# Kernel optimization log

Hardware: AMD Instinct MI355X
Metric: run time of the kernel (lower is better)

The kernel has to match this reference:

```python
import jax, jax.numpy as jnp
import numpy as np

N_IN, N_OUT, M, K, CIN, COUT = 262144, 393216, 262144, 27, 32, 64
BN_EPS = 1e-5


def setup_inputs() -> dict:
    key = jax.random.key(0)
    k0, k1, k2, k3 = jax.random.split(key, 4)
    data = jax.random.normal(k0, (N_IN, CIN), dtype=jnp.float32)
    # Kaiming-like scale for conv weights over K*Cin fan-in
    W = jax.random.normal(k1, (K, CIN, COUT), dtype=jnp.float32) * (1.0 / np.sqrt(K * CIN))
    gamma = jnp.ones((COUT,), dtype=jnp.float32)
    beta = jnp.zeros((COUT,), dtype=jnp.float32)
    in_idx = jax.random.randint(k2, (K, M), 0, N_IN, dtype=jnp.int32)
    out_idx = jax.random.randint(k3, (K, M), 0, N_OUT, dtype=jnp.int32)
    return {"data": data, "W": W, "gamma": gamma, "beta": beta,
            "in_idx": in_idx, "out_idx": out_idx}


def _sparse_conv(data, W, in_idx, out_idx):
    # Rulebook sparse conv: for each kernel offset k, gather -> matmul -> scatter-add.
    def step(acc, xs):
        in_i, out_i, Wk = xs              # [M], [M], [CIN, COUT]
        gathered = data[in_i]             # [M, CIN]
        contrib = gathered @ Wk           # [M, COUT]
        return acc.at[out_i].add(contrib), None

    out0 = jnp.zeros((N_OUT, COUT), dtype=data.dtype)
    out, _ = jax.lax.scan(step, out0, (in_idx, out_idx, W))
    return out


def _batch_norm(x, gamma, beta):
    # Sparse batch norm: per-channel stats over all active voxels (training mode).
    mean = jnp.mean(x, axis=0)
    var = jnp.var(x, axis=0)
    inv = jax.lax.rsqrt(var + BN_EPS)
    return (x - mean) * inv * gamma + beta


def reference(data, W, gamma, beta, in_idx, out_idx):
    conv_out = _sparse_conv(data, W, in_idx, out_idx)  # [N_OUT, COUT]
    return _batch_norm(conv_out, gamma, beta)
```

## Files before the change

### kernel.cpp

```cpp
#include <hip/hip_runtime.h>

#define N_IN   262144
#define N_OUT  393216
#define M_PAIRS 262144
#define KK     27
#define CIN    32
#define COUT   64
#define BN_EPS 1e-5f

#define BPK 256
#define PAIRS_PER_BLOCK (M_PAIRS / BPK)
#define CONV_BLOCK 256
#define WAVES_PER_BLOCK (CONV_BLOCK / 64)
#define PAIRS_PER_WAVE (PAIRS_PER_BLOCK / WAVES_PER_BLOCK)

__global__ __launch_bounds__(CONV_BLOCK) void conv_scatter(
    const float* __restrict__ data,
    const float* __restrict__ W,
    const int*   __restrict__ in_idx,
    const int*   __restrict__ out_idx,
    float*       __restrict__ out)
{
    __shared__ float Wlds[CIN * COUT];
    const int k   = blockIdx.x / BPK;
    const int blk = blockIdx.x % BPK;

    for (int i = threadIdx.x; i < CIN * COUT; i += CONV_BLOCK)
        Wlds[i] = W[k * CIN * COUT + i];
    __syncthreads();

    const int wave = threadIdx.x >> 6;
    const int lane = threadIdx.x & 63;
    const int base = k * M_PAIRS + blk * PAIRS_PER_BLOCK + wave * PAIRS_PER_WAVE;

    for (int p = 0; p < PAIRS_PER_WAVE; ++p) {
        const int in_i  = in_idx[base + p];
        const int out_i = out_idx[base + p];
        const float val = data[in_i * CIN + (lane & 31)];
        float acc = 0.0f;
        #pragma unroll
        for (int c = 0; c < CIN; ++c) {
            const float rowv = __shfl(val, c, 64);
            acc = fmaf(rowv, Wlds[c * COUT + lane], acc);
        }
        atomicAdd(&out[out_i * COUT + lane], acc);
    }
}

__global__ __launch_bounds__(256) void bn_stats(
    const float* __restrict__ out, float* __restrict__ stats )
{
    const int tid    = blockIdx.x * 256 + threadIdx.x;
    const int stride = gridDim.x * 256;
    float s = 0.0f, sq = 0.0f;
    const int total = N_OUT * COUT;
    for (int i = tid; i < total; i += stride) {
        const float x = out[i];
        s += x;
        sq += x * x;
    }
    __shared__ float ls[256], lsq[256];
    ls[threadIdx.x]  = s;
    lsq[threadIdx.x] = sq;
    __syncthreads();
    const int c = threadIdx.x;
    if (c < 64) {
        const float ts = ls[c] + ls[c + 64] + ls[c + 128] + ls[c + 192];
        const float tq = lsq[c] + lsq[c + 64] + lsq[c + 128] + lsq[c + 192];
        atomicAdd(&stats[c], ts);
        atomicAdd(&stats[64 + c], tq);
    }
}

__global__ __launch_bounds__(256) void bn_norm(
    float* __restrict__ out, const float* __restrict__ stats,
    const float* __restrict__ gamma, const float* __restrict__ beta)
{
    __shared__ float scale[COUT], bias[COUT];
    if (threadIdx.x < COUT) {
        const int c = threadIdx.x;
        const float invN = 1.0f / (float)N_OUT;
        const float mean = stats[c] * invN;
        const float var  = stats[64 + c] * invN - mean * mean;
        const float inv  = rsqrtf(var + BN_EPS);
        const float g    = gamma[c];
        scale[c] = inv * g;
        bias[c]  = beta[c] - mean * inv * g;
    }
    __syncthreads();

    const int tid    = blockIdx.x * blockDim.x + threadIdx.x;
    const int stride = gridDim.x * blockDim.x;
    const int total4 = N_OUT * COUT / 4;
    float4* o4 = (float4*)out;
    for (int i = tid; i < total4; i += stride) {
        float4 v = o4[i];
        const int c0 = (i * 4) & 63;
        v.x = v.x * scale[c0 + 0] + bias[c0 + 0];
        v.y = v.y * scale[c0 + 1] + bias[c0 + 1];
        v.z = v.z * scale[c0 + 2] + bias[c0 + 2];
        v.w = v.w * scale[c0 + 3] + bias[c0 + 3];
        o4[i] = v;
    }
}

extern "C" void kernel_launch(void* const* d_in, const int* in_sizes, int n_in,
                              void* d_out, int out_size, void* d_ws, size_t ws_size,
                              hipStream_t stream) {
    const float* data    = (const float*)d_in[0];
    const float* W       = (const float*)d_in[1];
    const float* gamma   = (const float*)d_in[2];
    const float* beta    = (const float*)d_in[3];
    const int*   in_idx  = (const int*)d_in[4];
    const int*   out_idx = (const int*)d_in[5];
    float* out   = (float*)d_out;
    float* stats = (float*)d_ws;

    hipMemsetAsync(d_out, 0, (size_t)N_OUT * COUT * sizeof(float), stream);
    hipMemsetAsync(d_ws, 0, 128 * sizeof(float), stream);

    conv_scatter<<<KK * BPK, CONV_BLOCK, 0, stream>>>(data, W, in_idx, out_idx, out);
    bn_stats<<<1024, 256, 0, stream>>>(out, stats);
    bn_norm<<<2048, 256, 0, stream>>>(out, stats, gamma, beta);
}
```

Before: 2.503 ms.

## Bin rulebook by output row range and accumulate in LDS with fused BN stats

Builds a counting-sort of rulebook entries keyed by (output row block, kernel offset): count, single-block prefix scan, then scatter packed records. Each block then owns 128 output rows, accumulates all contributions in shared memory with LDS atomics, computes BN partial statistics directly, and writes its tile once, removing global atomics, the output memset and the separate stats pass. The cost is extra passes over the index arrays, a serial one-block scan over about 80K bins, and only 3072 blocks with heavy LDS use. A fallback to the old path is kept for when the workspace is too small.

Measured after the change: 5.665 ms. 2.26x slower.

```diff
diff --git a/kernel.cpp b/kernel.cpp
--- a/kernel.cpp
+++ b/kernel.cpp
@@ -1,75 +1,139 @@
 #include <hip/hip_runtime.h>
 
-#define N_IN   262144
-#define N_OUT  393216
+#define N_IN    262144
+#define N_OUT   393216
 #define M_PAIRS 262144
-#define KK     27
-#define CIN    32
-#define COUT   64
-#define BN_EPS 1e-5f
-
-#define BPK 256
-#define PAIRS_PER_BLOCK (M_PAIRS / BPK)
-#define CONV_BLOCK 256
-#define WAVES_PER_BLOCK (CONV_BLOCK / 64)
-#define PAIRS_PER_WAVE (PAIRS_PER_BLOCK / WAVES_PER_BLOCK)
-
-__global__ __launch_bounds__(CONV_BLOCK) void conv_scatter(
+#define KK      27
+#define CIN     32
+#define COUT    64
+#define BN_EPS  1e-5f
+
+#define TOTAL_E      (KK * M_PAIRS)
+#define ROWS_PER_BIN 128
+#define NR           (N_OUT / ROWS_PER_BIN)
+#define NBINS        (NR * KK)
+
+typedef unsigned int u32;
+
+__global__ __launch_bounds__(256) void bin_count(
+    const int* __restrict__ out_idx, u32* __restrict__ cnt)
+{
+    const int stride = gridDim.x * 256;
+    for (int e = blockIdx.x * 256 + threadIdx.x; e < TOTAL_E; e += stride) {
+        const int k = e >> 18;
+        const int r = out_idx[e] >> 7;
+        atomicAdd(&cnt[r * KK + k], 1u);
+    }
+}
+
+__global__ __launch_bounds__(1024) void scan_bins(
+    u32* __restrict__ cnt, u32* __restrict__ off)
+{
+    __shared__ u32 sh[1024];
+    __shared__ u32 carry;
+    const int t = threadIdx.x;
+    if (t == 0) carry = 0;
+    __syncthreads();
+    for (int chunk = 0; chunk < NBINS / 1024; ++chunk) {
+        const int i = chunk * 1024 + t;
+        const u32 v = cnt[i];
+        sh[t] = v;
+        __syncthreads();
+        #pragma unroll
+        for (int d = 1; d < 1024; d <<= 1) {
+            const u32 add = (t >= d) ? sh[t - d] : 0u;
+            __syncthreads();
+            sh[t] += add;
+            __syncthreads();
+        }
+        const u32 excl = sh[t] - v + carry;
+        off[i] = excl;
+        cnt[i] = excl;
+        __syncthreads();
+        if (t == 1023) carry += sh[1023];
+        __syncthreads();
+    }
+    if (t == 0) off[NBINS] = carry;
+}
+
+__global__ __launch_bounds__(256) void bin_scatter(
+    const int* __restrict__ in_idx, const int* __restrict__ out_idx,
+    u32* __restrict__ cursor, u32* __restrict__ rec)
+{
+    const int stride = gridDim.x * 256;
+    for (int e = blockIdx.x * 256 + threadIdx.x; e < TOTAL_E; e += stride) {
+        const int k    = e >> 18;
+        const int oi   = out_idx[e];
+        const int ii   = in_idx[e];
+        const int bin  = (oi >> 7) * KK + k;
+        const u32 pos  = atomicAdd(&cursor[bin], 1u);
+        rec[pos] = (u32)ii | ((u32)(oi & 127) << 18);
+    }
+}
+
+__global__ __launch_bounds__(256) void range_accum(
     const float* __restrict__ data,
     const float* __restrict__ W,
-    const int*   __restrict__ in_idx,
-    const int*   __restrict__ out_idx,
-    float*       __restrict__ out)
-{
-    __shared__ float Wlds[CIN * COUT];
-    const int k   = blockIdx.x / BPK;
-    const int blk = blockIdx.x % BPK;
-
-    for (int i = threadIdx.x; i < CIN * COUT; i += CONV_BLOCK)
-        Wlds[i] = W[k * CIN * COUT + i];
-    __syncthreads();
-
-    const int wave = threadIdx.x >> 6;
-    const int lane = threadIdx.x & 63;
-    const int base = k * M_PAIRS + blk * PAIRS_PER_BLOCK + wave * PAIRS_PER_WAVE;
-
-    for (int p = 0; p < PAIRS_PER_WAVE; ++p) {
-        const int in_i  = in_idx[base + p];
-        const int out_i = out_idx[base + p];
-        const float val = data[in_i * CIN + (lane & 31)];
-        float acc = 0.0f;
-        #pragma unroll
-        for (int c = 0; c < CIN; ++c) {
-            const float rowv = __shfl(val, c, 64);
-            acc = fmaf(rowv, Wlds[c * COUT + lane], acc);
-        }
-        atomicAdd(&out[out_i * COUT + lane], acc);
-    }
-}
-
-__global__ __launch_bounds__(256) void bn_stats(
-    const float* __restrict__ out, float* __restrict__ stats )
-{
-    const int tid    = blockIdx.x * 256 + threadIdx.x;
-    const int stride = gridDim.x * 256;
-    float s = 0.0f, sq = 0.0f;
-    const int total = N_OUT * COUT;
-    for (int i = tid; i < total; i += stride) {
-        const float x = out[i];
-        s += x;
-        sq += x * x;
-    }
-    __shared__ float ls[256], lsq[256];
-    ls[threadIdx.x]  = s;
-    lsq[threadIdx.x] = sq;
-    __syncthreads();
-    const int c = threadIdx.x;
-    if (c < 64) {
-        const float ts = ls[c] + ls[c + 64] + ls[c + 128] + ls[c + 192];
-        const float tq = lsq[c] + lsq[c + 64] + lsq[c + 128] + lsq[c + 192];
-        atomicAdd(&stats[c], ts);
-        atomicAdd(&stats[64 + c], tq);
-    }
+    const u32*  __restrict__ off,
+    const u32*  __restrict__ rec,
+    float*      __restrict__ out,
+    float*      __restrict__ stats)
+{
+    __shared__ float acc[ROWS_PER_BIN * COUT];
+    __shared__ float Wl[CIN * COUT];
+    const int r    = blockIdx.x;
+    const int tid  = threadIdx.x;
+    const int wave = tid >> 6;
+    const int lane = tid & 63;
+
+    for (int i = tid; i < ROWS_PER_BIN * COUT; i += 256) acc[i] = 0.0f;
+
+    for (int k = 0; k < KK; ++k) {
+        __syncthreads();
+        for (int i = tid; i < CIN * COUT; i += 256)
+            Wl[i] = W[k * CIN * COUT + i];
+        __syncthreads();
+
+        const u32 begin = off[r * KK + k];
+        const u32 end   = off[r * KK + k + 1];
+        for (u32 idx = begin + wave; idx < end; idx += 4) {
+            const u32 rc   = rec[idx];
+            const int in_i = (int)(rc & 0x3FFFFu);
+            const int lo   = (int)(rc >> 18);
+            const float val = data[in_i * CIN + (lane & 31)];
+            float a = 0.0f;
+            #pragma unroll
+            for (int c = 0; c < CIN; ++c) {
+                const float rv = __shfl(val, c, 64);
+                a = fmaf(rv, Wl[c * COUT + lane], a);
+            }
+            atomicAdd(&acc[lo * COUT + lane], a);
+        }
+    }
+    __syncthreads();
+
+    {
+        const int c = tid & 63;
+        float s = 0.0f, sq = 0.0f;
+        for (int row = tid >> 6; row < ROWS_PER_BIN; row += 4) {
+            const float x = acc[row * COUT + c];
+            s += x; sq += x * x;
+        }
+        Wl[tid]       = s;
+        Wl[256 + tid] = sq;
+        __syncthreads();
+        if (tid < 64) {
+            const float ts = Wl[tid] + Wl[tid + 64] + Wl[tid + 128] + Wl[tid + 192];
+            const float tq = Wl[256 + tid] + Wl[320 + tid] + Wl[384 + tid] + Wl[448 + tid];
+            atomicAdd(&stats[tid], ts);
+            atomicAdd(&stats[64 + tid], tq);
+        }
+    }
+
+    const float4* a4 = (const float4*)acc;
+    float4* o4 = (float4*)out;
+    for (int i = tid; i < ROWS_PER_BIN * COUT / 4; i += 256)
+        o4[r * (ROWS_PER_BIN * COUT / 4) + i] = a4[i];
 }
 
 __global__ __launch_bounds__(256) void bn_norm(
@@ -104,6 +168,51 @@
     }
 }
 
+__global__ __launch_bounds__(256) void conv_scatter_fb(
+    const float* __restrict__ data, const float* __restrict__ W,
+    const int* __restrict__ in_idx, const int* __restrict__ out_idx,
+    float* __restrict__ out)
+{
+    __shared__ float Wlds[CIN * COUT];
+    const int k   = blockIdx.x / 256;
+    const int blk = blockIdx.x % 256;
+    for (int i = threadIdx.x; i < CIN * COUT; i += 256)
+        Wlds[i] = W[k * CIN * COUT + i];
+    __syncthreads();
+    const int wave = threadIdx.x >> 6;
+    const int lane = threadIdx.x & 63;
+    const int base = k * M_PAIRS + blk * 1024 + wave * 256;
+    for (int p = 0; p < 256; ++p) {
+        const int in_i  = in_idx[base + p];
+        const int out_i = out_idx[base + p];
+        const float val = data[in_i * CIN + (lane & 31)];
+        float a = 0.0f;
+        #pragma unroll
+        for (int c = 0; c < CIN; ++c)
+            a = fmaf(__shfl(val, c, 64), Wlds[c * COUT + lane], a);
+        atomicAdd(&out[out_i * COUT + lane], a);
+    }
+}
+
+__global__ __launch_bounds__(256) void bn_stats_fb(
+    const float* __restrict__ out, float* __restrict__ stats)
+{
+    const int tid    = blockIdx.x * 256 + threadIdx.x;
+    const int stride = gridDim.x * 256;
+    float s = 0.0f, sq = 0.0f;
+    for (int i = tid; i < N_OUT * COUT; i += stride) {
+        const float x = out[i]; s += x; sq += x * x;
+    }
+    __shared__ float ls[256], lsq[256];
+    ls[threadIdx.x] = s; lsq[threadIdx.x] = sq;
+    __syncthreads();
+    if (threadIdx.x < 64) {
+        const int c = threadIdx.x;
+        atomicAdd(&stats[c],      ls[c] + ls[c+64] + ls[c+128] + ls[c+192]);
+        atomicAdd(&stats[64 + c], lsq[c] + lsq[c+64] + lsq[c+128] + lsq[c+192]);
+    }
+}
+
 extern "C" void kernel_launch(void* const* d_in, const int* in_sizes, int n_in,
                               void* d_out, int out_size, void* d_ws, size_t ws_size,
                               hipStream_t stream) {
@@ -113,13 +222,29 @@
     const float* beta    = (const float*)d_in[3];
     const int*   in_idx  = (const int*)d_in[4];
     const int*   out_idx = (const int*)d_in[5];
-    float* out   = (float*)d_out;
-    float* stats = (float*)d_ws;
-
-    hipMemsetAsync(d_out, 0, (size_t)N_OUT * COUT * sizeof(float), stream);
-    hipMemsetAsync(d_ws, 0, 128 * sizeof(float), stream);
-
-    conv_scatter<<<KK * BPK, CONV_BLOCK, 0, stream>>>(data, W, in_idx, out_idx, out);
-    bn_stats<<<1024, 256, 0, stream>>>(out, stats);
-    bn_norm<<<2048, 256, 0, stream>>>(out, stats, gamma, beta);
-}
+    float* out = (float*)d_out;
+
+    u32* cnt = (u32*)d_ws;
+    u32* off = cnt + NBINS;
+    u32* rec = off + NBINS + 1;
+    float* stats = (float*)(rec + TOTAL_E);
+    const size_t ws_needed = (size_t)(NBINS + NBINS + 1 + TOTAL_E + 128) * 4;
+
+    if (ws_size >= ws_needed) {
+        hipMemsetAsync(cnt, 0, (size_t)NBINS * sizeof(u32), stream);
+        hipMemsetAsync(stats, 0, 128 * sizeof(float), stream);
+
+        bin_count<<<4096, 256, 0, stream>>>(out_idx, cnt);
+        scan_bins<<<1, 1024, 0, stream>>>(cnt, off);
+        bin_scatter<<<4096, 256, 0, stream>>>(in_idx, out_idx, cnt, rec);
+        range_accum<<<NR, 256, 0, stream>>>(data, W, off, rec, out, stats);
+        bn_norm<<<2048, 256, 0, stream>>>(out, stats, gamma, beta);
+    } else {
+        float* stats_fb = (float*)d_ws;
+        hipMemsetAsync(d_out, 0, (size_t)N_OUT * COUT * sizeof(float), stream);
+        hipMemsetAsync(stats_fb, 0, 128 * sizeof(float), stream);
+        conv_scatter_fb<<<KK * 256, 256, 0, stream>>>(data, W, in_idx, out_idx, out);
+        bn_stats_fb<<<1024, 256, 0, stream>>>(out, stats_fb);
+        bn_norm<<<2048, 256, 0, stream>>>(out, stats_fb, gamma, beta);
+    }
+}
```

## Accumulate conv scatter in packed bf16 atomics with bf16 workspace for BN

Applied to the files above, without the earlier changes.

The conv scatter now packs pairs of adjacent output channels into bf16x2 and uses global_atomic_pk_add_bf16 into a bf16 workspace buffer, halving the number of atomics and the accumulator footprint. BN stats and normalization read the bf16 buffer and write fp32 output. The aim is to cut atomic traffic and memory bandwidth, but accumulating up to ~27 contributions in bf16 loses substantial precision and may fail tolerance. A fallback fp32 path is kept for when the workspace is too small.

After: 3.227 ms. +28.9%, slower.

```diff
diff --git a/kernel.cpp b/kernel.cpp
--- a/kernel.cpp
+++ b/kernel.cpp
@@ -1,25 +1,42 @@
 #include <hip/hip_runtime.h>
-
-#define N_IN   262144
-#define N_OUT  393216
+#include <hip/hip_bf16.h>
+
+#define N_IN    262144
+#define N_OUT   393216
 #define M_PAIRS 262144
-#define KK     27
-#define CIN    32
-#define COUT   64
-#define BN_EPS 1e-5f
+#define KK      27
+#define CIN     32
+#define COUT    64
+#define BN_EPS  1e-5f
 
 #define BPK 256
-#define PAIRS_PER_BLOCK (M_PAIRS / BPK)
 #define CONV_BLOCK 256
-#define WAVES_PER_BLOCK (CONV_BLOCK / 64)
-#define PAIRS_PER_WAVE (PAIRS_PER_BLOCK / WAVES_PER_BLOCK)
-
-__global__ __launch_bounds__(CONV_BLOCK) void conv_scatter(
+
+typedef unsigned int u32;
+
+static __device__ __forceinline__ u32 pack_bf2(float lo, float hi) {
+    __hip_bfloat16 a = __float2bfloat16(lo);
+    __hip_bfloat16 b = __float2bfloat16(hi);
+    return (u32)*reinterpret_cast<unsigned short*>(&a)
+         | ((u32)*reinterpret_cast<unsigned short*>(&b) << 16);
+}
+
+static __device__ __forceinline__ float bfbits2f(u32 bits16) {
+    return __uint_as_float(bits16 << 16);
+}
+
+static __device__ __forceinline__ void atomic_pk_add_bf16(u32* addr, u32 packed) {
+    asm volatile("global_atomic_pk_add_bf16 %0, %1, off"
+                 :: "v"((void*)addr), "v"(packed)
+                 : "memory");
+}
+
+__global__ __launch_bounds__(CONV_BLOCK) void conv_scatter_pk(
     const float* __restrict__ data,
     const float* __restrict__ W,
     const int*   __restrict__ in_idx,
     const int*   __restrict__ out_idx,
-    float*       __restrict__ out)
+    u32*         __restrict__ outbf)
 {
     __shared__ float Wlds[CIN * COUT];
     const int k   = blockIdx.x / BPK;
@@ -31,9 +48,9 @@
 
     const int wave = threadIdx.x >> 6;
     const int lane = threadIdx.x & 63;
-    const int base = k * M_PAIRS + blk * PAIRS_PER_BLOCK + wave * PAIRS_PER_WAVE;
-
-    for (int p = 0; p < PAIRS_PER_WAVE; ++p) {
+    const int base = k * M_PAIRS + blk * 1024 + wave * 256;
+
+    for (int p = 0; p < 256; ++p) {
         const int in_i  = in_idx[base + p];
         const int out_i = out_idx[base + p];
         const float val = data[in_i * CIN + (lane & 31)];
@@ -43,38 +60,47 @@
             const float rowv = __shfl(val, c, 64);
             acc = fmaf(rowv, Wlds[c * COUT + lane], acc);
         }
-        atomicAdd(&out[out_i * COUT + lane], acc);
-    }
-}
-
-__global__ __launch_bounds__(256) void bn_stats(
-    const float* __restrict__ out, float* __restrict__ stats )
-{
+        const float accN = __shfl(acc, lane ^ 1, 64);
+        if (!(lane & 1)) {
+            atomic_pk_add_bf16(&outbf[out_i * 32 + (lane >> 1)],
+                               pack_bf2(acc, accN));
+        }
+    }
+}
+
+__global__ __launch_bounds__(256) void bn_stats_bf(
+    const u32* __restrict__ outbf, float* __restrict__ stats )
+{
+    __shared__ float s_[256];
+    s_[threadIdx.x] = 0.0f;
+    __syncthreads();
+
     const int tid    = blockIdx.x * 256 + threadIdx.x;
     const int stride = gridDim.x * 256;
-    float s = 0.0f, sq = 0.0f;
-    const int total = N_OUT * COUT;
-    for (int i = tid; i < total; i += stride) {
-        const float x = out[i];
-        s += x;
-        sq += x * x;
-    }
-    __shared__ float ls[256], lsq[256];
-    ls[threadIdx.x]  = s;
-    lsq[threadIdx.x] = sq;
-    __syncthreads();
-    const int c = threadIdx.x;
-    if (c < 64) {
-        const float ts = ls[c] + ls[c + 64] + ls[c + 128] + ls[c + 192];
-        const float tq = lsq[c] + lsq[c + 64] + lsq[c + 128] + lsq[c + 192];
-        atomicAdd(&stats[c], ts);
-        atomicAdd(&stats[64 + c], tq);
-    }
-}
-
-__global__ __launch_bounds__(256) void bn_norm(
-    float* __restrict__ out, const float* __restrict__ stats,
-    const float* __restrict__ gamma, const float* __restrict__ beta)
+    const int j      = threadIdx.x & 31;
+    float s0 = 0.f, q0 = 0.f, s1 = 0.f, q1 = 0.f;
+    for (int i = tid; i < N_OUT * 32; i += stride) {
+        const u32 v = outbf[i];
+        const float x0 = bfbits2f(v & 0xFFFFu);
+        const float x1 = bfbits2f(v >> 16);
+        s0 += x0; q0 += x0 * x0;
+        s1 += x1; q1 += x1 * x1;
+    }
+    atomicAdd(&s_[2 * j],           s0);
+    atomicAdd(&s_[2 * j + 1],       s1);
+    atomicAdd(&s_[128 + 2 * j],     q0);
+    atomicAdd(&s_[128 + 2 * j + 1], q1);
+    __syncthreads();
+    if (threadIdx.x < 64) {
+        atomicAdd(&stats[threadIdx.x],      s_[threadIdx.x]);
+        atomicAdd(&stats[64 + threadIdx.x], s_[128 + threadIdx.x]);
+    }
+}
+
+__global__ __launch_bounds__(256) void bn_norm_bf(
+    const u32* __restrict__ outbf, const float* __restrict__ stats,
+    const float* __restrict__ gamma, const float* __restrict__ beta,
+    float* __restrict__ out)
 {
     __shared__ float scale[COUT], bias[COUT];
     if (threadIdx.x < COUT) {
@@ -91,9 +117,82 @@
 
     const int tid    = blockIdx.x * blockDim.x + threadIdx.x;
     const int stride = gridDim.x * blockDim.x;
-    const int total4 = N_OUT * COUT / 4;
+    float2* o2 = (float2*)out;
+    for (int i = tid; i < N_OUT * 32; i += stride) {
+        const u32 v = outbf[i];
+        const int c0 = (i & 31) * 2;
+        float2 r;
+        r.x = bfbits2f(v & 0xFFFFu) * scale[c0]     + bias[c0];
+        r.y = bfbits2f(v >> 16)     * scale[c0 + 1] + bias[c0 + 1];
+        o2[i] = r;
+    }
+}
+
+__global__ __launch_bounds__(CONV_BLOCK) void conv_scatter_fb(
+    const float* __restrict__ data, const float* __restrict__ W,
+    const int* __restrict__ in_idx, const int* __restrict__ out_idx,
+    float* __restrict__ out)
+{
+    __shared__ float Wlds[CIN * COUT];
+    const int k   = blockIdx.x / BPK;
+    const int blk = blockIdx.x % BPK;
+    for (int i = threadIdx.x; i < CIN * COUT; i += CONV_BLOCK)
+        Wlds[i] = W[k * CIN * COUT + i];
+    __syncthreads();
+    const int wave = threadIdx.x >> 6;
+    const int lane = threadIdx.x & 63;
+    const int base = k * M_PAIRS + blk * 1024 + wave * 256;
+    for (int p = 0; p < 256; ++p) {
+        const int in_i  = in_idx[base + p];
+        const int out_i = out_idx[base + p];
+        const float val = data[in_i * CIN + (lane & 31)];
+        float acc = 0.0f;
+        #pragma unroll
+        for (int c = 0; c < CIN; ++c)
+            acc = fmaf(__shfl(val, c, 64), Wlds[c * COUT + lane], acc);
+        atomicAdd(&out[out_i * COUT + lane], acc);
+    }
+}
+
+__global__ __launch_bounds__(256) void bn_stats_fb(
+    const float* __restrict__ out, float* __restrict__ stats)
+{
+    const int tid    = blockIdx.x * 256 + threadIdx.x;
+    const int stride = gridDim.x * 256;
+    float s = 0.0f, sq = 0.0f;
+    for (int i = tid; i < N_OUT * COUT; i += stride) {
+        const float x = out[i]; s += x; sq += x * x;
+    }
+    __shared__ float ls[256], lsq[256];
+    ls[threadIdx.x] = s; lsq[threadIdx.x] = sq;
+    __syncthreads();
+    if (threadIdx.x < 64) {
+        const int c = threadIdx.x;
+        atomicAdd(&stats[c],      ls[c] + ls[c+64] + ls[c+128] + ls[c+192]);
+        atomicAdd(&stats[64 + c], lsq[c] + lsq[c+64] + lsq[c+128] + lsq[c+192]);
+    }
+}
+
+__global__ __launch_bounds__(256) void bn_norm_fb(
+    float* __restrict__ out, const float* __restrict__ stats,
+    const float* __restrict__ gamma, const float* __restrict__ beta)
+{
+    __shared__ float scale[COUT], bias[COUT];
+    if (threadIdx.x < COUT) {
+        const int c = threadIdx.x;
+        const float invN = 1.0f / (float)N_OUT;
+        const float mean = stats[c] * invN;
+        const float var  = stats[64 + c] * invN - mean * mean;
+        const float inv  = rsqrtf(var + BN_EPS);
+        const float g    = gamma[c];
+        scale[c] = inv * g;
+        bias[c]  = beta[c] - mean * inv * g;
+    }
+    __syncthreads();
+    const int tid    = blockIdx.x * blockDim.x + threadIdx.x;
+    const int stride = gridDim.x * blockDim.x;
     float4* o4 = (float4*)out;
-    for (int i = tid; i < total4; i += stride) {
+    for (int i = tid; i < N_OUT * COUT / 4; i += stride) {
         float4 v = o4[i];
         const int c0 = (i * 4) & 63;
         v.x = v.x * scale[c0 + 0] + bias[c0 + 0];
@@ -113,13 +212,27 @@
     const float* beta    = (const float*)d_in[3];
     const int*   in_idx  = (const int*)d_in[4];
     const int*   out_idx = (const int*)d_in[5];
-    float* out   = (float*)d_out;
-    float* stats = (float*)d_ws;
-
-    hipMemsetAsync(d_out, 0, (size_t)N_OUT * COUT * sizeof(float), stream);
-    hipMemsetAsync(d_ws, 0, 128 * sizeof(float), stream);
-
-    conv_scatter<<<KK * BPK, CONV_BLOCK, 0, stream>>>(data, W, in_idx, out_idx, out);
-    bn_stats<<<1024, 256, 0, stream>>>(out, stats);
-    bn_norm<<<2048, 256, 0, stream>>>(out, stats, gamma, beta);
-}
+    float* out = (float*)d_out;
+
+    u32*   outbf = (u32*)d_ws;
+    float* stats = (float*)(outbf + (size_t)N_OUT * 32);
+    const size_t needed = (size_t)N_OUT * 32 * 4 + 128 * 4;
+
+    if (ws_size >= needed) {
+        hipMemsetAsync(outbf, 0, (size_t)N_OUT * 32 * sizeof(u32), stream);
+        hipMemsetAsync(stats, 0, 128 * sizeof(float), stream);
+
+        conv_scatter_pk<<<KK * BPK, CONV_BLOCK, 0, stream>>>(
+            data, W, in_idx, out_idx, outbf);
+        bn_stats_bf<<<1024, 256, 0, stream>>>(outbf, stats);
+        bn_norm_bf<<<2048, 256, 0, stream>>>(outbf, stats, gamma, beta, out);
+    } else {
+        float* stats_fb = (float*)d_ws;
+        hipMemsetAsync(d_out, 0, (size_t)N_OUT * COUT * sizeof(float), stream);
+        hipMemsetAsync(stats_fb, 0, 128 * sizeof(float), stream);
+        conv_scatter_fb<<<KK * BPK, CONV_BLOCK, 0, stream>>>(
+            data, W, in_idx, out_idx, out);
+        bn_stats_fb<<<1024, 256, 0, stream>>>(out, stats_fb);
+        bn_norm_fb<<<2048, 256, 0, stream>>>(out, stats_fb, gamma, beta);
+    }
+}
```
